# Optimization experiments

Hardware: AMD Instinct MI355X
Metric: run time of the kernel (lower is better)

## Reference

```python
import jax, jax.numpy as jnp
import numpy as np

B, C, H, Wd = 4, 64, 64, 64


def setup_inputs() -> dict:
    key = jax.random.key(0)
    k1, k2, k3 = jax.random.split(key, 3)
    x = jax.random.normal(k1, (B, C, H, Wd), dtype=jnp.float32)
    W = jax.random.normal(k2, (C, C), dtype=jnp.float32) * (1.0 / np.sqrt(C))
    b = jax.random.normal(k3, (C,), dtype=jnp.float32) * 0.01
    return {"x": x, "W": W, "b": b}


def reference(x, W, b):
    Bz, Cz, Hz, Wz = x.shape
    N = Hz * Wz
    xf = x.reshape(Bz, Cz, N)                      # values [B,C,N]
    # shared 1x1 conv for queries and keys (same module instance in torch)
    qk = jnp.einsum('oc,bcn->bon', W, xf) + b[None, :, None]  # [B,C,N]
    # scores[b,n,m] = sum_c q[b,c,n] * k[b,c,m], scaled by 1/N
    scores = jnp.einsum('bcn,bcm->bnm', qk, qk) / N           # [B,N,N]
    attn = jax.nn.softmax(scores, axis=-1)                    # softmax over m
    # out[b,c,n] = sum_m values[b,c,m] * attn[b,n,m]
    out = jnp.einsum('bcm,bnm->bcn', xf, attn)
    return out.reshape(Bz, Cz, Hz, Wz)
```

## Files before the change

kernel.cpp:

```cpp
#include <hip/hip_runtime.h>
#include <hip/hip_bf16.h>

#define BATCH 4
#define NSP   4096

typedef __bf16 bf16x8v __attribute__((ext_vector_type(8)));
typedef __bf16 bf16x4v __attribute__((ext_vector_type(4)));
typedef float  floatx4 __attribute__((ext_vector_type(4)));
typedef short  shortx4 __attribute__((ext_vector_type(4)));

#if defined(__HIP_DEVICE_COMPILE__)
#  if __has_builtin(__builtin_amdgcn_mfma_f32_16x16x16bf16_1k)
static __device__ inline floatx4 mfma16(bf16x4v a, bf16x4v b, floatx4 c) {
    return __builtin_amdgcn_mfma_f32_16x16x16bf16_1k(
        __builtin_bit_cast(shortx4, a), __builtin_bit_cast(shortx4, b), c, 0, 0, 0);
}
#  elif __has_builtin(__builtin_amdgcn_mfma_f32_16x16x16_bf16)
static __device__ inline floatx4 mfma16(bf16x4v a, bf16x4v b, floatx4 c) {
    return __builtin_amdgcn_mfma_f32_16x16x16_bf16(a, b, c, 0, 0, 0);
}
#  else
#    error "gfx950 device pass should have a K=16 bf16 mfma builtin"
#  endif
#else
static __device__ inline floatx4 mfma16(bf16x4v, bf16x4v, floatx4 c) { return c; }
#endif

__global__ __launch_bounds__(256) void qk_kernel(const float* __restrict__ x,
                                                 const float* __restrict__ Wm,
                                                 const float* __restrict__ bias,
                                                 __bf16* __restrict__ qkT) {
    __shared__ __align__(16) __bf16 xT[64 * 72];

    const int t  = threadIdx.x;
    const int b  = blockIdx.x >> 6;
    const int n0 = (blockIdx.x & 63) << 6;

#pragma unroll
    for (int p = 0; p < 4; ++p) {
        const int c  = p * 16 + (t >> 4);
        const int n4 = (t & 15) * 4;
        const float4 v = *(const float4*)(x + (size_t)(b * 64 + c) * 4096 + n0 + n4);
        xT[(n4 + 0) * 72 + c] = (__bf16)(v.x * 0.015625f);
        xT[(n4 + 1) * 72 + c] = (__bf16)(v.y * 0.015625f);
        xT[(n4 + 2) * 72 + c] = (__bf16)(v.z * 0.015625f);
        xT[(n4 + 3) * 72 + c] = (__bf16)(v.w * 0.015625f);
    }
    __syncthreads();

    const int w = t >> 6, lane = t & 63, quad = lane >> 4, l16 = lane & 15;
    const bf16x8v a0 = *(const bf16x8v*)(xT + (w * 16 + l16) * 72 + quad * 8);
    const bf16x8v a1 = *(const bf16x8v*)(xT + (w * 16 + l16) * 72 + 32 + quad * 8);

    floatx4 acc[4];
#pragma unroll
    for (int ot = 0; ot < 4; ++ot) {
        const float* wr = Wm + (ot * 16 + l16) * 64;
        float4 wa = *(const float4*)(wr + quad * 8);
        float4 wb = *(const float4*)(wr + quad * 8 + 4);
        float4 wc = *(const float4*)(wr + 32 + quad * 8);
        float4 wd = *(const float4*)(wr + 32 + quad * 8 + 4);
        bf16x8v b0, b1;
        b0[0]=(__bf16)wa.x; b0[1]=(__bf16)wa.y; b0[2]=(__bf16)wa.z; b0[3]=(__bf16)wa.w;
        b0[4]=(__bf16)wb.x; b0[5]=(__bf16)wb.y; b0[6]=(__bf16)wb.z; b0[7]=(__bf16)wb.w;
        b1[0]=(__bf16)wc.x; b1[1]=(__bf16)wc.y; b1[2]=(__bf16)wc.z; b1[3]=(__bf16)wc.w;
        b1[4]=(__bf16)wd.x; b1[5]=(__bf16)wd.y; b1[6]=(__bf16)wd.z; b1[7]=(__bf16)wd.w;
        acc[ot] = floatx4{0.f, 0.f, 0.f, 0.f};
        acc[ot] = __builtin_amdgcn_mfma_f32_16x16x32_bf16(a0, b0, acc[ot], 0, 0, 0);
        acc[ot] = __builtin_amdgcn_mfma_f32_16x16x32_bf16(a1, b1, acc[ot], 0, 0, 0);
    }
    __syncthreads();

#pragma unroll
    for (int ot = 0; ot < 4; ++ot) {
        const float bo = bias[ot * 16 + l16] * 0.015625f;
#pragma unroll
        for (int r = 0; r < 4; ++r)
            xT[(w * 16 + quad * 4 + r) * 72 + ot * 16 + l16] = (__bf16)(acc[ot][r] + bo);
    }
    __syncthreads();

    const int n = t >> 2, seg = t & 3;
    __bf16* dst = qkT + (size_t)(b * 4096 + n0 + n) * 64 + seg * 16;
    *(bf16x8v*)dst       = *(const bf16x8v*)(xT + n * 72 + seg * 16);
    *(bf16x8v*)(dst + 8) = *(const bf16x8v*)(xT + n * 72 + seg * 16 + 8);
}

#define BUFB 18432

template<int SPLIT, int ITERS>
__global__ __launch_bounds__(256, 4) void attn_kernel(const float* __restrict__ x,
                                                      const __bf16* __restrict__ qkT,
                                                      __bf16* __restrict__ Opart,
                                                      float* __restrict__ Lpart) {
    __shared__ __align__(16) char smem[36864];
    float* Olds = (float*)smem;

    const int t   = threadIdx.x;
    const int blk = blockIdx.x;
    const int xcd = blk & 7;
    const int b   = xcd >> 1;
    const int sub = ((blk >> 3) << 1) | (xcd & 1);
    const int qt  = sub / SPLIT;
    const int s   = sub % SPLIT;
    const int n0  = qt << 7;
    const int pblk = (b * 32 + qt) * SPLIT + s;

    const int w = t >> 6, lane = t & 63, quad = lane >> 4, l16 = lane & 15;

    bf16x8v fq[2][2];
#pragma unroll
    for (int qt2 = 0; qt2 < 2; ++qt2) {
        const __bf16* qrow = qkT + (size_t)(b * 4096 + n0 + w * 32 + qt2 * 16 + l16) * 64;
        fq[qt2][0] = *(const bf16x8v*)(qrow + quad * 8);
        fq[qt2][1] = *(const bf16x8v*)(qrow + 32 + quad * 8);
    }

    floatx4 oacc[2][4];
#pragma unroll
    for (int i = 0; i < 2; ++i)
#pragma unroll
        for (int j = 0; j < 4; ++j) oacc[i][j] = floatx4{0.f, 0.f, 0.f, 0.f};
    float rs[2] = {0.f, 0.f};

    const int krow = t >> 3, kc8 = (t & 7) * 8;
    const int vc   = t >> 4, vk  = t & 15;
    const int vj   = (vk & 3) * 16 + (vk >> 2) * 4;
    const __bf16* kgp = qkT + (size_t)b * 4096 * 64 + (size_t)s * (64 * ITERS) * 64;
    const float*  vgp = x + (size_t)b * 64 * 4096 + s * (64 * ITERS);

    uint4  kpre[2];
    float4 vpre[4];
#pragma unroll
    for (int i = 0; i < 2; ++i)
        kpre[i] = *(const uint4*)(kgp + (size_t)(krow + i * 32) * 64 + kc8);
#pragma unroll
    for (int i = 0; i < 4; ++i)
        vpre[i] = *(const float4*)(vgp + (size_t)(vc + i * 16) * 4096 + vk * 4);

    for (int it = 0; it < ITERS; ++it) {
        __bf16* Kb = (__bf16*)(smem + (it & 1) * BUFB);
        __bf16* Vb = (__bf16*)(smem + (it & 1) * BUFB + 9216);

#pragma unroll
        for (int i = 0; i < 2; ++i)
            *(uint4*)(Kb + (krow + i * 32) * 72 + kc8) = kpre[i];
#pragma unroll
        for (int i = 0; i < 4; ++i) {
            bf16x4v bv;
            bv[0] = (__bf16)vpre[i].x; bv[1] = (__bf16)vpre[i].y;
            bv[2] = (__bf16)vpre[i].z; bv[3] = (__bf16)vpre[i].w;
            *(bf16x4v*)(Vb + (vc + i * 16) * 72 + vj) = bv;
        }
        __syncthreads();

        if (it + 1 < ITERS) {
            const int m1 = (it + 1) << 6;
#pragma unroll
            for (int i = 0; i < 2; ++i)
                kpre[i] = *(const uint4*)(kgp + (size_t)(m1 + krow + i * 32) * 64 + kc8);
#pragma unroll
            for (int i = 0; i < 4; ++i)
                vpre[i] = *(const float4*)(vgp + (size_t)(vc + i * 16) * 4096 + m1 + vk * 4);
        }

        bf16x4v pf[4][2];
#pragma unroll
        for (int mt = 0; mt < 4; ++mt) {
            const __bf16* kr = Kb + (mt * 16 + l16) * 72;
            bf16x8v ak0 = *(const bf16x8v*)(kr + quad * 8);
            bf16x8v ak1 = *(const bf16x8v*)(kr + 32 + quad * 8);
#pragma unroll
            for (int qt2 = 0; qt2 < 2; ++qt2) {
                floatx4 sT = {0.f, 0.f, 0.f, 0.f};
                sT = __builtin_amdgcn_mfma_f32_16x16x32_bf16(ak0, fq[qt2][0], sT, 0, 0, 0);
                sT = __builtin_amdgcn_mfma_f32_16x16x32_bf16(ak1, fq[qt2][1], sT, 0, 0, 0);
                float p0 = __expf(sT[0]), p1 = __expf(sT[1]);
                float p2 = __expf(sT[2]), p3 = __expf(sT[3]);
                rs[qt2] += (p0 + p1) + (p2 + p3);
                bf16x4v pv;
                pv[0] = (__bf16)p0; pv[1] = (__bf16)p1; pv[2] = (__bf16)p2; pv[3] = (__bf16)p3;
                pf[mt][qt2] = pv;
            }
        }

#pragma unroll
        for (int ct = 0; ct < 4; ++ct) {
            const __bf16* vb = Vb + (ct * 16 + l16) * 72 + quad * 16;
            bf16x8v v01 = *(const bf16x8v*)vb;
            bf16x8v v23 = *(const bf16x8v*)(vb + 8);
            bf16x4v av0 = {v01[0], v01[1], v01[2], v01[3]};
            bf16x4v av1 = {v01[4], v01[5], v01[6], v01[7]};
            bf16x4v av2 = {v23[0], v23[1], v23[2], v23[3]};
            bf16x4v av3 = {v23[4], v23[5], v23[6], v23[7]};
#pragma unroll
            for (int qt2 = 0; qt2 < 2; ++qt2) {
                oacc[qt2][ct] = mfma16(av0, pf[0][qt2], oacc[qt2][ct]);
                oacc[qt2][ct] = mfma16(av1, pf[1][qt2], oacc[qt2][ct]);
                oacc[qt2][ct] = mfma16(av2, pf[2][qt2], oacc[qt2][ct]);
                oacc[qt2][ct] = mfma16(av3, pf[3][qt2], oacc[qt2][ct]);
            }
        }
    }

#pragma unroll
    for (int qt2 = 0; qt2 < 2; ++qt2) {
        float v = rs[qt2];
        v += __shfl_xor(v, 16, 64);
        v += __shfl_xor(v, 32, 64);
        if (quad == 0)
            Lpart[(size_t)pblk * 128 + w * 32 + qt2 * 16 + l16] = v;
    }

    __syncthreads();

#pragma unroll
    for (int qt2 = 0; qt2 < 2; ++qt2)
#pragma unroll
        for (int ct = 0; ct < 4; ++ct)
#pragma unroll
            for (int r = 0; r < 4; ++r)
                Olds[(ct * 16 + quad * 4 + r) * 132 + w * 32 + qt2 * 16 + l16] = oacc[qt2][ct][r];
    __syncthreads();

    const int c = t >> 2, seg = t & 3;
#pragma unroll
    for (int i = 0; i < 4; ++i) {
        floatx4 v0 = *(const floatx4*)(Olds + c * 132 + seg * 32 + i * 8);
        floatx4 v1 = *(const floatx4*)(Olds + c * 132 + seg * 32 + i * 8 + 4);
        bf16x8v pk;
        pk[0]=(__bf16)v0[0]; pk[1]=(__bf16)v0[1]; pk[2]=(__bf16)v0[2]; pk[3]=(__bf16)v0[3];
        pk[4]=(__bf16)v1[0]; pk[5]=(__bf16)v1[1]; pk[6]=(__bf16)v1[2]; pk[7]=(__bf16)v1[3];
        *(bf16x8v*)(Opart + (size_t)pblk * 8192 + c * 128 + seg * 32 + i * 8) = pk;
    }
}

template<int SPLIT>
__global__ __launch_bounds__(256) void reduce_kernel(const __bf16* __restrict__ Opart,
                                                     const float* __restrict__ Lpart,
                                                     float* __restrict__ out) {
    __shared__ float linv[128];
    const int blk = blockIdx.x;
    const int bq = blk >> 2, cq = blk & 3;
    const int b = bq >> 5, qt = bq & 31;
    const int t = threadIdx.x;

    if (t < 128) {
        float sl = 0.f;
#pragma unroll
        for (int s = 0; s < SPLIT; ++s)
            sl += Lpart[((size_t)bq * SPLIT + s) * 128 + t];
        linv[t] = 1.0f / sl;
    }
    __syncthreads();

    const int c  = cq * 16 + (t >> 4);
    const int q8 = (t & 15) * 8;

    float a[8] = {0.f,0.f,0.f,0.f,0.f,0.f,0.f,0.f};
#pragma unroll
    for (int s = 0; s < SPLIT; ++s) {
        bf16x8v v = *(const bf16x8v*)(Opart + ((size_t)bq * SPLIT + s) * 8192 + c * 128 + q8);
#pragma unroll
        for (int k = 0; k < 8; ++k) a[k] += (float)v[k];
    }
    float* op = out + (size_t)(b * 64 + c) * 4096 + qt * 128 + q8;
    float4 o0, o1;
    o0.x = a[0]*linv[q8+0]; o0.y = a[1]*linv[q8+1]; o0.z = a[2]*linv[q8+2]; o0.w = a[3]*linv[q8+3];
    o1.x = a[4]*linv[q8+4]; o1.y = a[5]*linv[q8+5]; o1.z = a[6]*linv[q8+6]; o1.w = a[7]*linv[q8+7];
    *(float4*)op       = o0;
    *(float4*)(op + 4) = o1;
}

extern "C" void kernel_launch(void* const* d_in, const int* in_sizes, int n_in,
                              void* d_out, int out_size, void* d_ws, size_t ws_size,
                              hipStream_t stream) {
    const float* x    = (const float*)d_in[0];
    const float* Wm   = (const float*)d_in[1];
    const float* bias = (const float*)d_in[2];
    float* out = (float*)d_out;

    char* ws = (char*)d_ws;
    __bf16* qkT = (__bf16*)ws;

    qk_kernel<<<BATCH * (NSP / 64), 256, 0, stream>>>(x, Wm, bias, qkT);

    const size_t QKT = 2097152;
    const size_t needBig = QKT + (size_t)1024 * 8192 * 2 + (size_t)1024 * 128 * 4;
    if (ws_size >= needBig) {
        __bf16* Opart = (__bf16*)(ws + QKT);
        float*  Lpart = (float*)(ws + QKT + (size_t)1024 * 8192 * 2);
        attn_kernel<8, 8><<<BATCH * 32 * 8, 256, 0, stream>>>(x, qkT, Opart, Lpart);
        reduce_kernel<8><<<512, 256, 0, stream>>>(Opart, Lpart, out);
    } else {
        __bf16* Opart = (__bf16*)(ws + QKT);
        float*  Lpart = (float*)(ws + QKT + (size_t)512 * 8192 * 2);
        attn_kernel<4, 16><<<BATCH * 32 * 4, 256, 0, stream>>>(x, qkT, Opart, Lpart);
        reduce_kernel<4><<<512, 256, 0, stream>>>(Opart, Lpart, out);
    }
}
```

Before: 101.8 us.

## Pre-convert values to bf16 in qk kernel and fold log2e into QK scale

```diff
diff --git a/kernel.cpp b/kernel.cpp
--- a/kernel.cpp
+++ b/kernel.cpp
@@ -3,6 +3,8 @@
 
 #define BATCH 4
 #define NSP   4096
+
+#define QKSCALE 0.01876754f
 
 typedef __bf16 bf16x8v __attribute__((ext_vector_type(8)));
 typedef __bf16 bf16x4v __attribute__((ext_vector_type(4)));
@@ -29,7 +31,8 @@
 __global__ __launch_bounds__(256) void qk_kernel(const float* __restrict__ x,
                                                  const float* __restrict__ Wm,
                                                  const float* __restrict__ bias,
-                                                 __bf16* __restrict__ qkT) {
+                                                 __bf16* __restrict__ qkT,
+                                                 __bf16* __restrict__ xb) {
     __shared__ __align__(16) __bf16 xT[64 * 72];
 
     const int t  = threadIdx.x;
@@ -41,10 +44,13 @@
         const int c  = p * 16 + (t >> 4);
         const int n4 = (t & 15) * 4;
         const float4 v = *(const float4*)(x + (size_t)(b * 64 + c) * 4096 + n0 + n4);
-        xT[(n4 + 0) * 72 + c] = (__bf16)(v.x * 0.015625f);
-        xT[(n4 + 1) * 72 + c] = (__bf16)(v.y * 0.015625f);
-        xT[(n4 + 2) * 72 + c] = (__bf16)(v.z * 0.015625f);
-        xT[(n4 + 3) * 72 + c] = (__bf16)(v.w * 0.015625f);
+        xT[(n4 + 0) * 72 + c] = (__bf16)(v.x * QKSCALE);
+        xT[(n4 + 1) * 72 + c] = (__bf16)(v.y * QKSCALE);
+        xT[(n4 + 2) * 72 + c] = (__bf16)(v.z * QKSCALE);
+        xT[(n4 + 3) * 72 + c] = (__bf16)(v.w * QKSCALE);
+        bf16x4v xu;
+        xu[0] = (__bf16)v.x; xu[1] = (__bf16)v.y; xu[2] = (__bf16)v.z; xu[3] = (__bf16)v.w;
+        *(bf16x4v*)(xb + (size_t)(b * 64 + c) * 4096 + n0 + n4) = xu;
     }
     __syncthreads();
 
@@ -73,7 +79,7 @@
 
 #pragma unroll
     for (int ot = 0; ot < 4; ++ot) {
-        const float bo = bias[ot * 16 + l16] * 0.015625f;
+        const float bo = bias[ot * 16 + l16] * QKSCALE;
 #pragma unroll
         for (int r = 0; r < 4; ++r)
             xT[(w * 16 + quad * 4 + r) * 72 + ot * 16 + l16] = (__bf16)(acc[ot][r] + bo);
@@ -89,7 +95,7 @@
 #define BUFB 18432
 
 template<int SPLIT, int ITERS>
-__global__ __launch_bounds__(256, 4) void attn_kernel(const float* __restrict__ x,
+__global__ __launch_bounds__(256, 4) void attn_kernel(const __bf16* __restrict__ xb,
                                                       const __bf16* __restrict__ qkT,
                                                       __bf16* __restrict__ Opart,
                                                       float* __restrict__ Lpart) {
@@ -124,44 +130,41 @@
     float rs[2] = {0.f, 0.f};
 
     const int krow = t >> 3, kc8 = (t & 7) * 8;
-    const int vc   = t >> 4, vk  = t & 15;
-    const int vj   = (vk & 3) * 16 + (vk >> 2) * 4;
+    const int vc   = t >> 3, vh  = t & 7;
+    const int vjlo = (((2 * vh) & 3) * 16) + (((2 * vh) >> 2) * 4);
+    const int vjhi = (((2 * vh + 1) & 3) * 16) + (((2 * vh + 1) >> 2) * 4);
     const __bf16* kgp = qkT + (size_t)b * 4096 * 64 + (size_t)s * (64 * ITERS) * 64;
-    const float*  vgp = x + (size_t)b * 64 * 4096 + s * (64 * ITERS);
-
-    uint4  kpre[2];
-    float4 vpre[4];
-#pragma unroll
-    for (int i = 0; i < 2; ++i)
+    const __bf16* vgp = xb + (size_t)b * 64 * 4096 + s * (64 * ITERS);
+
+    uint4 kpre[2];
+    uint4 vpre[2];
+#pragma unroll
+    for (int i = 0; i < 2; ++i) {
         kpre[i] = *(const uint4*)(kgp + (size_t)(krow + i * 32) * 64 + kc8);
-#pragma unroll
-    for (int i = 0; i < 4; ++i)
-        vpre[i] = *(const float4*)(vgp + (size_t)(vc + i * 16) * 4096 + vk * 4);
+        vpre[i] = *(const uint4*)(vgp + (size_t)(vc + i * 32) * 4096 + vh * 8);
+    }
 
     for (int it = 0; it < ITERS; ++it) {
         __bf16* Kb = (__bf16*)(smem + (it & 1) * BUFB);
         __bf16* Vb = (__bf16*)(smem + (it & 1) * BUFB + 9216);
 
 #pragma unroll
-        for (int i = 0; i < 2; ++i)
+        for (int i = 0; i < 2; ++i) {
             *(uint4*)(Kb + (krow + i * 32) * 72 + kc8) = kpre[i];
-#pragma unroll
-        for (int i = 0; i < 4; ++i) {
-            bf16x4v bv;
-            bv[0] = (__bf16)vpre[i].x; bv[1] = (__bf16)vpre[i].y;
-            bv[2] = (__bf16)vpre[i].z; bv[3] = (__bf16)vpre[i].w;
-            *(bf16x4v*)(Vb + (vc + i * 16) * 72 + vj) = bv;
+            uint2 lo = {vpre[i].x, vpre[i].y};
+            uint2 hi = {vpre[i].z, vpre[i].w};
+            *(uint2*)(Vb + (vc + i * 32) * 72 + vjlo) = lo;
+            *(uint2*)(Vb + (vc + i * 32) * 72 + vjhi) = hi;
         }
         __syncthreads();
 
         if (it + 1 < ITERS) {
             const int m1 = (it + 1) << 6;
 #pragma unroll
-            for (int i = 0; i < 2; ++i)
+            for (int i = 0; i < 2; ++i) {
                 kpre[i] = *(const uint4*)(kgp + (size_t)(m1 + krow + i * 32) * 64 + kc8);
-#pragma unroll
-            for (int i = 0; i < 4; ++i)
-                vpre[i] = *(const float4*)(vgp + (size_t)(vc + i * 16) * 4096 + m1 + vk * 4);
+                vpre[i] = *(const uint4*)(vgp + (size_t)(vc + i * 32) * 4096 + m1 + vh * 8);
+            }
         }
 
         bf16x4v pf[4][2];
@@ -175,8 +178,8 @@
                 floatx4 sT = {0.f, 0.f, 0.f, 0.f};
                 sT = __builtin_amdgcn_mfma_f32_16x16x32_bf16(ak0, fq[qt2][0], sT, 0, 0, 0);
                 sT = __builtin_amdgcn_mfma_f32_16x16x32_bf16(ak1, fq[qt2][1], sT, 0, 0, 0);
-                float p0 = __expf(sT[0]), p1 = __expf(sT[1]);
-                float p2 = __expf(sT[2]), p3 = __expf(sT[3]);
+                float p0 = exp2f(sT[0]), p1 = exp2f(sT[1]);
+                float p2 = exp2f(sT[2]), p3 = exp2f(sT[3]);
                 rs[qt2] += (p0 + p1) + (p2 + p3);
                 bf16x4v pv;
                 pv[0] = (__bf16)p0; pv[1] = (__bf16)p1; pv[2] = (__bf16)p2; pv[3] = (__bf16)p3;
@@ -282,20 +285,21 @@
 
     char* ws = (char*)d_ws;
     __bf16* qkT = (__bf16*)ws;
-
-    qk_kernel<<<BATCH * (NSP / 64), 256, 0, stream>>>(x, Wm, bias, qkT);
-
-    const size_t QKT = 2097152;
-    const size_t needBig = QKT + (size_t)1024 * 8192 * 2 + (size_t)1024 * 128 * 4;
+    __bf16* xb  = (__bf16*)(ws + 2097152);
+    const size_t HDR = 4194304;
+
+    qk_kernel<<<BATCH * (NSP / 64), 256, 0, stream>>>(x, Wm, bias, qkT, xb);
+
+    const size_t needBig = HDR + (size_t)1024 * 8192 * 2 + (size_t)1024 * 128 * 4;
     if (ws_size >= needBig) {
-        __bf16* Opart = (__bf16*)(ws + QKT);
-        float*  Lpart = (float*)(ws + QKT + (size_t)1024 * 8192 * 2);
-        attn_kernel<8, 8><<<BATCH * 32 * 8, 256, 0, stream>>>(x, qkT, Opart, Lpart);
+        __bf16* Opart = (__bf16*)(ws + HDR);
+        float*  Lpart = (float*)(ws + HDR + (size_t)1024 * 8192 * 2);
+        attn_kernel<8, 8><<<BATCH * 32 * 8, 256, 0, stream>>>(xb, qkT, Opart, Lpart);
         reduce_kernel<8><<<512, 256, 0, stream>>>(Opart, Lpart, out);
     } else {
-        __bf16* Opart = (__bf16*)(ws + QKT);
-        float*  Lpart = (float*)(ws + QKT + (size_t)512 * 8192 * 2);
-        attn_kernel<4, 16><<<BATCH * 32 * 4, 256, 0, stream>>>(x, qkT, Opart, Lpart);
+        __bf16* Opart = (__bf16*)(ws + HDR);
+        float*  Lpart = (float*)(ws + HDR + (size_t)512 * 8192 * 2);
+        attn_kernel<4, 16><<<BATCH * 32 * 4, 256, 0, stream>>>(xb, qkT, Opart, Lpart);
         reduce_kernel<4><<<512, 256, 0, stream>>>(Opart, Lpart, out);
     }
 }
```

Measured after the change: 106.8 us. 5.0% more time.
